# Performance work log

Hardware: AMD Instinct MI355X
Metric: run time of the kernel (lower is better)

## Reference

```python
import jax, jax.numpy as jnp
import numpy as np

IN_FEATURES = 4096
OUT_FEATURES = 4096
OUTLIER_NUM = 128
Q_IN = IN_FEATURES - OUTLIER_NUM  # 3968
B, S = 4, 2048


def _build_perm(seed=0):
    rng = np.random.default_rng(seed)
    outlier_ids = rng.choice(IN_FEATURES, size=OUTLIER_NUM, replace=False)
    mask = np.ones(IN_FEATURES, dtype=bool)
    mask[outlier_ids] = False
    col_ids = np.arange(IN_FEATURES, dtype=np.int32)
    col_perm = np.concatenate([col_ids[mask], col_ids[~mask]])
    inv_col_perm = np.zeros(IN_FEATURES, dtype=np.int32)
    inv_col_perm[col_perm] = np.arange(IN_FEATURES, dtype=np.int32)
    return inv_col_perm


def setup_inputs() -> dict:
    key = jax.random.key(0)
    k1, k2, k3, k4, k5 = jax.random.split(key, 5)
    inp = {
        "input": jax.random.normal(k1, (B, S, IN_FEATURES), dtype=jnp.float32),
        # low-bit integer codes stored as float (e.g. int4 range), per-row scale
        "q_weight": jax.random.randint(k2, (OUT_FEATURES, Q_IN), -8, 8).astype(jnp.float32),
        "fp_weight": jax.random.normal(k3, (OUT_FEATURES, OUTLIER_NUM), dtype=jnp.float32),
        "alpha_scale": jax.random.uniform(k4, (OUT_FEATURES, 1), dtype=jnp.float32, minval=0.01, maxval=0.1),
        "bias": jax.random.normal(k5, (OUT_FEATURES,), dtype=jnp.float32),
        "inv_col_perm": jnp.asarray(_build_perm(), dtype=jnp.int32),
    }
    return inp


def reference(input, q_weight, fp_weight, alpha_scale, bias, inv_col_perm):
    # SymQuant.dequantize: per-output-row symmetric scale
    dq_w = q_weight * alpha_scale                      # [O, Q_IN]
    out_w = jnp.concatenate([dq_w, fp_weight], axis=1)  # [O, IN]
    out_w = out_w[:, inv_col_perm]                      # undo column permutation
    # F.linear: input @ out_w.T + bias
    return jnp.einsum("bsi,oi->bso", input, out_w) + bias
```

## Files before the change

kernel.cpp:

```cpp
#include <hip/hip_runtime.h>
#include <stdint.h>

#define IN_F  4096
#define OUT_F 4096
#define OUTL  128
#define QIN   (IN_F - OUTL)
#define MTOT  8192
#define BM 128
#define BN 128
#define BKB 128

typedef unsigned short u16;
typedef int i32x4 __attribute__((ext_vector_type(4)));

#define QPAD(j) ((j) + (((j) >> 5) << 2))

__global__ __launch_bounds__(256) void prep_fused(
    const float* __restrict__ A, signed char* __restrict__ A8,
    float* __restrict__ s_arr,
    const float* __restrict__ qw, const float* __restrict__ fpw,
    const float* __restrict__ alpha, const int* __restrict__ invp,
    signed char* __restrict__ W8, float* __restrict__ t_arr) {
  const int tid = threadIdx.x;
  __shared__ float red[4];

  if (blockIdx.x >= OUT_F) {
    const int m = blockIdx.x - OUT_F;
    const float* row = A + (size_t)m * IN_F;
    float4 v[4];
    float amax = 0.f;
#pragma unroll
    for (int k = 0; k < 4; ++k) {
      v[k] = ((const float4*)row)[k * 256 + tid];
      amax = fmaxf(amax, fmaxf(fmaxf(fabsf(v[k].x), fabsf(v[k].y)),
                               fmaxf(fabsf(v[k].z), fabsf(v[k].w))));
    }
#pragma unroll
    for (int off = 32; off; off >>= 1)
      amax = fmaxf(amax, __shfl_xor(amax, off, 64));
    if ((tid & 63) == 0) red[tid >> 6] = amax;
    __syncthreads();
    amax = fmaxf(fmaxf(red[0], red[1]), fmaxf(red[2], red[3]));
    const float inv = 127.f / amax;
    if (tid == 0) s_arr[m] = amax / 127.f;
#pragma unroll
    for (int k = 0; k < 4; ++k) {
      const int q0 = __float2int_rn(v[k].x * inv);
      const int q1 = __float2int_rn(v[k].y * inv);
      const int q2 = __float2int_rn(v[k].z * inv);
      const int q3 = __float2int_rn(v[k].w * inv);
      const uint32_t p = (q0 & 255) | ((q1 & 255) << 8) |
                         ((q2 & 255) << 16) | ((uint32_t)(q3 & 255) << 24);
      ((uint32_t*)A8)[(size_t)m * (IN_F / 4) + k * 256 + tid] = p;
    }
  } else {
    const int o = blockIdx.x;
    __shared__ float qs[QIN + ((QIN >> 5) << 2)];
    __shared__ float fs[OUTL];

    int4 jj[4];
#pragma unroll
    for (int q = 0; q < 4; ++q) jj[q] = ((const int4*)invp)[tid * 4 + q];

    const float a = alpha[o];
    float amax = 0.f;

    float4 f;
    if (tid < OUTL / 4) f = ((const float4*)(fpw + (size_t)o * OUTL))[tid];

    const float4* qrow = (const float4*)(qw + (size_t)o * QIN);
#pragma unroll
    for (int k = 0; k < 4; ++k) {
      const int idx = k * 256 + tid;
      if (idx < QIN / 4) {
        const float4 q = qrow[idx];
        ((float4*)&qs[idx * 4 + ((idx >> 3) << 2)])[0] = q;
        const float qm = fmaxf(fmaxf(fabsf(q.x), fabsf(q.y)),
                               fmaxf(fabsf(q.z), fabsf(q.w)));
        amax = fmaxf(amax, qm * a);
      }
    }
    if (tid < OUTL / 4) {
      ((float4*)fs)[tid] = f;
      amax = fmaxf(amax, fmaxf(fmaxf(fabsf(f.x), fabsf(f.y)),
                               fmaxf(fabsf(f.z), fabsf(f.w))));
    }
#pragma unroll
    for (int off = 32; off; off >>= 1)
      amax = fmaxf(amax, __shfl_xor(amax, off, 64));
    if ((tid & 63) == 0) red[tid >> 6] = amax;
    __syncthreads();
    amax = fmaxf(fmaxf(red[0], red[1]), fmaxf(red[2], red[3]));
    const float invws = 127.f / amax;
    if (tid == 0) t_arr[o] = amax / 127.f;

    signed char vals[16];
#pragma unroll
    for (int q = 0; q < 4; ++q) {
      const int j[4] = {jj[q].x, jj[q].y, jj[q].z, jj[q].w};
#pragma unroll
      for (int e = 0; e < 4; ++e) {
        const int je = j[e];
        const float v = (je < QIN) ? qs[QPAD(je)] * a : fs[je - QIN];
        vals[q * 4 + e] = (signed char)__float2int_rn(v * invws);
      }
    }
    ((uint4*)(W8 + (size_t)o * IN_F))[tid] = *(const uint4*)vals;
  }
}

#define GLDS(g, l)                                                              \
  __builtin_amdgcn_global_load_lds(                                             \
      (const __attribute__((address_space(1))) void*)(g),                       \
      (__attribute__((address_space(3))) void*)(l), 16, 0, 0)

__global__ __launch_bounds__(256, 3) void gemm_i8(
    const signed char* __restrict__ A8, const signed char* __restrict__ W8,
    const float* __restrict__ s_arr, const float* __restrict__ t_arr,
    const float* __restrict__ bias, float* __restrict__ C) {
  __shared__ unsigned char As8[BM * BKB];
  __shared__ unsigned char Bs8[BN * BKB];

  const int tid  = threadIdx.x;
  const int wave = tid >> 6;
  const int lane = tid & 63;
  const int bn = blockIdx.x, bm = blockIdx.y;
  const int wm = (wave >> 1) * 64;
  const int wn = (wave & 1)  * 64;

  const int srow   = wave * 32 + (lane >> 3);
  const int schunk = (lane & 7) ^ ((lane >> 3) & 7);
  const signed char* Ag = A8 + (size_t)(bm * BM + srow) * IN_F + schunk * 16;
  const signed char* Wg = W8 + (size_t)(bn * BN + srow) * IN_F + schunk * 16;
  unsigned char* AsW = As8 + wave * 32 * BKB;
  unsigned char* BsW = Bs8 + wave * 32 * BKB;

  i32x4 acc[4][4];
#pragma unroll
  for (int mi = 0; mi < 4; ++mi)
#pragma unroll
    for (int ni = 0; ni < 4; ++ni) acc[mi][ni] = (i32x4){0, 0, 0, 0};

  const int fr = lane & 15;
  const int fq = lane >> 4;

  for (int kt = 0; kt < IN_F / BKB; ++kt) {
    __syncthreads();
#pragma unroll
    for (int t = 0; t < 4; ++t) {
      GLDS(Ag + kt * BKB + t * 8 * IN_F, AsW + t * 8 * BKB);
      GLDS(Wg + kt * BKB + t * 8 * IN_F, BsW + t * 8 * BKB);
    }
    __syncthreads();

#pragma unroll
    for (int ks = 0; ks < 2; ++ks) {
      i32x4 af[4], bg[4];
#pragma unroll
      for (int mi = 0; mi < 4; ++mi)
        af[mi] = *(const i32x4*)
            &As8[(wm + mi * 16 + fr) * BKB + (((ks * 4 + fq) ^ (fr & 7)) * 16)];
#pragma unroll
      for (int ni = 0; ni < 4; ++ni)
        bg[ni] = *(const i32x4*)
            &Bs8[(wn + ni * 16 + fr) * BKB + (((ks * 4 + fq) ^ (fr & 7)) * 16)];
#pragma unroll
      for (int mi = 0; mi < 4; ++mi)
#pragma unroll
        for (int ni = 0; ni < 4; ++ni)
          acc[mi][ni] = __builtin_amdgcn_mfma_i32_16x16x64_i8(
              af[mi], bg[ni], acc[mi][ni], 0, 0, 0);
    }
  }

  float sv[4][4];
#pragma unroll
  for (int mi = 0; mi < 4; ++mi)
#pragma unroll
    for (int rr = 0; rr < 4; ++rr)
      sv[mi][rr] = s_arr[bm * BM + wm + mi * 16 + fq * 4 + rr];

#pragma unroll
  for (int ni = 0; ni < 4; ++ni) {
    const int n = bn * BN + wn + ni * 16 + fr;
    const float tn = t_arr[n];
    const float bv = bias[n];
#pragma unroll
    for (int mi = 0; mi < 4; ++mi) {
      const int m0 = bm * BM + wm + mi * 16 + fq * 4;
#pragma unroll
      for (int rr = 0; rr < 4; ++rr)
        C[(size_t)(m0 + rr) * OUT_F + n] =
            (float)acc[mi][ni][rr] * (sv[mi][rr] * tn) + bv;
    }
  }
}

extern "C" void kernel_launch(void* const* d_in, const int* in_sizes, int n_in,
                              void* d_out, int out_size, void* d_ws, size_t ws_size,
                              hipStream_t stream) {
  const float* input = (const float*)d_in[0];
  const float* qw    = (const float*)d_in[1];
  const float* fpw   = (const float*)d_in[2];
  const float* alpha = (const float*)d_in[3];
  const float* bias  = (const float*)d_in[4];
  const int*   invp  = (const int*)d_in[5];

  char* ws = (char*)d_ws;
  signed char* A8    = (signed char*)ws;
  signed char* W8    = (signed char*)(ws + (32ull << 20));
  float* s_arr = (float*)(ws + (48ull << 20));
  float* t_arr = (float*)(ws + (48ull << 20) + (64ull << 10));
  float* out = (float*)d_out;

  prep_fused<<<OUT_F + MTOT, 256, 0, stream>>>(input, A8, s_arr, qw, fpw,
                                               alpha, invp, W8, t_arr);

  dim3 ggrid(OUT_F / BN, MTOT / BM);
  gemm_i8<<<ggrid, dim3(256), 0, stream>>>(A8, W8, s_arr, t_arr, bias, out);
}
```

Before: 397.9 us.

## Use 256x256 tiles, 512 threads, double-buffered LDS with interleaved load/MFMA schedule

Grows the GEMM block tile to 256x256 with 8 waves, each computing a 128x64 sub-tile, which raises operand reuse per LDS load. LDS is split into double buffers with 64-byte K halves, so global-to-LDS loads for the next K tile are issued between MFMA phases, with explicit barriers, vmcnt waits and setprio to overlap memory and compute. The cost is more accumulator registers, fewer blocks (512 total) and a hand-ordered schedule that is fragile and relies on exact waitcnt counts.

```diff
diff --git a/kernel.cpp b/kernel.cpp
--- a/kernel.cpp
+++ b/kernel.cpp
@@ -6,9 +6,10 @@
 #define OUTL  128
 #define QIN   (IN_F - OUTL)
 #define MTOT  8192
-#define BM 128
-#define BN 128
+#define BM 256
+#define BN 256
 #define BKB 128
+#define NKT (IN_F / BKB)
 
 typedef unsigned short u16;
 typedef int i32x4 __attribute__((ext_vector_type(4)));
@@ -114,68 +115,137 @@
       (const __attribute__((address_space(1))) void*)(g),                       \
       (__attribute__((address_space(3))) void*)(l), 16, 0, 0)
 
-__global__ __launch_bounds__(256, 3) void gemm_i8(
+#define BAR()                                                                   \
+  do {                                                                          \
+    __builtin_amdgcn_sched_barrier(0);                                          \
+    __builtin_amdgcn_s_barrier();                                               \
+    __builtin_amdgcn_sched_barrier(0);                                          \
+  } while (0)
+
+__global__ __launch_bounds__(512, 2) void gemm_i8(
     const signed char* __restrict__ A8, const signed char* __restrict__ W8,
     const float* __restrict__ s_arr, const float* __restrict__ t_arr,
     const float* __restrict__ bias, float* __restrict__ C) {
-  __shared__ unsigned char As8[BM * BKB];
-  __shared__ unsigned char Bs8[BN * BKB];
+  __shared__ unsigned char As[2][2][256 * 64];
+  __shared__ unsigned char Bs[2][2][256 * 64];
 
   const int tid  = threadIdx.x;
   const int wave = tid >> 6;
   const int lane = tid & 63;
   const int bn = blockIdx.x, bm = blockIdx.y;
-  const int wm = (wave >> 1) * 64;
-  const int wn = (wave & 1)  * 64;
-
-  const int srow   = wave * 32 + (lane >> 3);
-  const int schunk = (lane & 7) ^ ((lane >> 3) & 7);
+
+  const int wm = (wave >> 2) * 128;
+  const int wn = (wave & 3) * 64;
+
+  const int srow   = wave * 32 + (lane >> 2);
+  const int schunk = (lane & 3) ^ ((lane >> 3) & 3);
   const signed char* Ag = A8 + (size_t)(bm * BM + srow) * IN_F + schunk * 16;
   const signed char* Wg = W8 + (size_t)(bn * BN + srow) * IN_F + schunk * 16;
-  unsigned char* AsW = As8 + wave * 32 * BKB;
-  unsigned char* BsW = Bs8 + wave * 32 * BKB;
-
-  i32x4 acc[4][4];
-#pragma unroll
-  for (int mi = 0; mi < 4; ++mi)
+  const int stg = wave * 32 * 64;
+
+  i32x4 acc[8][4];
+#pragma unroll
+  for (int mi = 0; mi < 8; ++mi)
 #pragma unroll
     for (int ni = 0; ni < 4; ++ni) acc[mi][ni] = (i32x4){0, 0, 0, 0};
 
   const int fr = lane & 15;
   const int fq = lane >> 4;
-
-  for (int kt = 0; kt < IN_F / BKB; ++kt) {
-    __syncthreads();
-#pragma unroll
-    for (int t = 0; t < 4; ++t) {
-      GLDS(Ag + kt * BKB + t * 8 * IN_F, AsW + t * 8 * BKB);
-      GLDS(Wg + kt * BKB + t * 8 * IN_F, BsW + t * 8 * BKB);
-    }
-    __syncthreads();
-
-#pragma unroll
-    for (int ks = 0; ks < 2; ++ks) {
-      i32x4 af[4], bg[4];
-#pragma unroll
-      for (int mi = 0; mi < 4; ++mi)
-        af[mi] = *(const i32x4*)
-            &As8[(wm + mi * 16 + fr) * BKB + (((ks * 4 + fq) ^ (fr & 7)) * 16)];
+  const int cswz = (fq ^ ((fr >> 1) & 3)) * 16;
+
+  int aoff[8], boff[4];
+#pragma unroll
+  for (int mi = 0; mi < 8; ++mi) aoff[mi] = (wm + mi * 16 + fr) * 64 + cswz;
+#pragma unroll
+  for (int ni = 0; ni < 4; ++ni) boff[ni] = (wn + ni * 16 + fr) * 64 + cswz;
+
+  auto LDA = [&](int buf, int ks, int half, i32x4* af) {
+#pragma unroll
+    for (int mi = 0; mi < 4; ++mi)
+      af[mi] = *(const i32x4*)&As[buf][ks][aoff[half * 4 + mi]];
+  };
+  auto LDB = [&](int buf, int ks, i32x4* bg) {
+#pragma unroll
+    for (int ni = 0; ni < 4; ++ni)
+      bg[ni] = *(const i32x4*)&Bs[buf][ks][boff[ni]];
+  };
+  auto MM = [&](int mh, const i32x4* af, const i32x4* bg) {
+    __builtin_amdgcn_s_setprio(1);
+#pragma unroll
+    for (int mi = 0; mi < 4; ++mi)
 #pragma unroll
       for (int ni = 0; ni < 4; ++ni)
-        bg[ni] = *(const i32x4*)
-            &Bs8[(wn + ni * 16 + fr) * BKB + (((ks * 4 + fq) ^ (fr & 7)) * 16)];
-#pragma unroll
-      for (int mi = 0; mi < 4; ++mi)
-#pragma unroll
-        for (int ni = 0; ni < 4; ++ni)
-          acc[mi][ni] = __builtin_amdgcn_mfma_i32_16x16x64_i8(
-              af[mi], bg[ni], acc[mi][ni], 0, 0, 0);
-    }
-  }
-
-  float sv[4][4];
-#pragma unroll
-  for (int mi = 0; mi < 4; ++mi)
+        acc[mh * 4 + mi][ni] = __builtin_amdgcn_mfma_i32_16x16x64_i8(
+            af[mi], bg[ni], acc[mh * 4 + mi][ni], 0, 0, 0);
+    __builtin_amdgcn_s_setprio(0);
+  };
+  auto STG = [&](int nbuf, int op , int ks, int ktn) {
+    const signed char* g = (op ? Wg : Ag) + ktn * BKB + ks * 64;
+    unsigned char* d = op ? &Bs[nbuf][ks][stg] : &As[nbuf][ks][stg];
+    GLDS(g, d);
+    GLDS(g + 16 * IN_F, d + 1024);
+  };
+
+  STG(0, 0, 0, 0);
+  STG(0, 1, 0, 0);
+  STG(0, 0, 1, 0);
+  STG(0, 1, 1, 0);
+  asm volatile("s_waitcnt vmcnt(0)" ::: "memory");
+  BAR();
+
+  for (int kt = 0; kt < NKT - 1; ++kt) {
+    const int buf = kt & 1, nbuf = buf ^ 1;
+    i32x4 af[4], bg[4];
+    LDA(buf, 0, 0, af);
+    LDB(buf, 0, bg);
+    STG(nbuf, 0, 0, kt + 1);
+    BAR();
+    MM(0, af, bg);
+    BAR();
+    LDA(buf, 0, 1, af);
+    STG(nbuf, 1, 0, kt + 1);
+    BAR();
+    MM(1, af, bg);
+    asm volatile("s_waitcnt vmcnt(4)" ::: "memory");
+    BAR();
+    LDA(buf, 1, 0, af);
+    LDB(buf, 1, bg);
+    STG(nbuf, 0, 1, kt + 1);
+    BAR();
+    MM(0, af, bg);
+    BAR();
+    LDA(buf, 1, 1, af);
+    STG(nbuf, 1, 1, kt + 1);
+    BAR();
+    MM(1, af, bg);
+    asm volatile("s_waitcnt vmcnt(4)" ::: "memory");
+    BAR();
+  }
+  {
+    i32x4 af[4], bg[4];
+    LDA(1, 0, 0, af);
+    LDB(1, 0, bg);
+    BAR();
+    MM(0, af, bg);
+    BAR();
+    LDA(1, 0, 1, af);
+    BAR();
+    MM(1, af, bg);
+    asm volatile("s_waitcnt vmcnt(0)" ::: "memory");
+    BAR();
+    LDA(1, 1, 0, af);
+    LDB(1, 1, bg);
+    BAR();
+    MM(0, af, bg);
+    BAR();
+    LDA(1, 1, 1, af);
+    BAR();
+    MM(1, af, bg);
+  }
+
+  float sv[8][4];
+#pragma unroll
+  for (int mi = 0; mi < 8; ++mi)
 #pragma unroll
     for (int rr = 0; rr < 4; ++rr)
       sv[mi][rr] = s_arr[bm * BM + wm + mi * 16 + fq * 4 + rr];
@@ -186,7 +256,7 @@
     const float tn = t_arr[n];
     const float bv = bias[n];
 #pragma unroll
-    for (int mi = 0; mi < 4; ++mi) {
+    for (int mi = 0; mi < 8; ++mi) {
       const int m0 = bm * BM + wm + mi * 16 + fq * 4;
 #pragma unroll
       for (int rr = 0; rr < 4; ++rr)
@@ -217,5 +287,5 @@
                                                alpha, invp, W8, t_arr);
 
   dim3 ggrid(OUT_F / BN, MTOT / BM);
-  gemm_i8<<<ggrid, dim3(256), 0, stream>>>(A8, W8, s_arr, t_arr, bias, out);
+  gemm_i8<<<ggrid, dim3(512), 0, stream>>>(A8, W8, s_arr, t_arr, bias, out);
 }
```

Result: slower. 436.1 us (+9.6%).
